# Kernel tuning notes

Hardware: AMD Instinct MI355X
Metric: run time of the kernel (lower is better)

Reference implementation:

```python
import jax, jax.numpy as jnp
import numpy as np

LN_EPS = 1e-5  # torch LayerNorm default
K_NN = 5       # top-5 nearest patterns (simple-surprise path)


def setup_inputs() -> dict:
    key = jax.random.key(0)
    ks = jax.random.split(key, 5)
    B, S, D, M = 8, 8192, 256, 50
    return {
        "hidden_states": jax.random.normal(ks[0], (B, S, D), dtype=jnp.float32),
        "memory": jax.random.normal(ks[1], (M, D), dtype=jnp.float32),
        "W1": jax.random.normal(ks[2], (D, 2 * D), dtype=jnp.float32) * (1.0 / np.sqrt(D)),
        "b1": jnp.zeros((2 * D,), dtype=jnp.float32),
        "W2": jax.random.normal(ks[3], (2 * D, D), dtype=jnp.float32) * (1.0 / np.sqrt(2 * D)),
        "b2": jnp.zeros((D,), dtype=jnp.float32),
        "ln_gamma": jnp.ones((D,), dtype=jnp.float32),
        "ln_beta": jnp.zeros((D,), dtype=jnp.float32),
    }


def reference(hidden_states, memory, W1, b1, W2, b2, ln_gamma, ln_beta):
    # Feature extractor: Linear -> ReLU -> (Dropout, eval=identity) -> Linear -> LayerNorm
    h = jax.nn.relu(jnp.einsum("bsd,de->bse", hidden_states, W1) + b1)
    f = jnp.einsum("bse,ed->bsd", h, W2) + b2
    mu = jnp.mean(f, axis=-1, keepdims=True)
    var = jnp.var(f, axis=-1, keepdims=True)
    feats = (f - mu) * jax.lax.rsqrt(var + LN_EPS) * ln_gamma + ln_beta  # [B,S,D]

    # Simple-surprise path, vectorized over all (b, s) tokens:
    # L2 distance of each token feature to every memory pattern.
    f_sq = jnp.sum(feats * feats, axis=-1)      # [B,S]
    m_sq = jnp.sum(memory * memory, axis=-1)    # [M]
    dots = jnp.einsum("bsd,md->bsm", feats, memory)  # [B,S,M]
    d2 = jnp.maximum(f_sq[..., None] + m_sq - 2.0 * dots, 0.0)
    dists = jnp.sqrt(d2)                        # [B,S,M]

    # k smallest distances -> mean -> sigmoid(avg - 1)
    neg_knn, _ = jax.lax.top_k(-dists, K_NN)    # [B,S,K]
    avg_dist = -jnp.mean(neg_knn, axis=-1)      # [B,S]
    surprise_scores = jax.nn.sigmoid(avg_dist - 1.0)
    return surprise_scores
```

## Files before the change

kernel.cpp:

```cpp
#include <hip/hip_runtime.h>
#include <math.h>

typedef __attribute__((ext_vector_type(8))) short bf16x8;
typedef __attribute__((ext_vector_type(4))) float f32x4;

static __device__ __forceinline__ unsigned short f2b(float x) {
  unsigned int u = __float_as_uint(x);
  u += 0x7FFFu + ((u >> 16) & 1u);
  return (unsigned short)(u >> 16);
}

__global__ void prep_weights(const float* __restrict__ W1,
                             const float* __restrict__ W2,
                             const float* __restrict__ mem,
                             unsigned short* __restrict__ W1T,
                             unsigned short* __restrict__ W2T,
                             unsigned short* __restrict__ memB,
                             float* __restrict__ msq) {
  int i = blockIdx.x * 256 + threadIdx.x;
  if (i < 131072) {
    int k = i >> 9, n = i & 511;
    W1T[n * 256 + k] = f2b(W1[i]);
  } else if (i < 262144) {
    int j = i - 131072;
    int k = j >> 8, n = j & 255;
    W2T[n * 512 + k] = f2b(W2[j]);
  } else if (i < 278528) {
    int j = i - 262144;
    int r = j >> 8;
    memB[j] = (r < 50) ? f2b(mem[j]) : (unsigned short)0;
  } else {
    int t = threadIdx.x;
    int r = t >> 2, c0 = (t & 3) * 64;
    float s = 0.f;
    if (r < 50) {
      for (int c = 0; c < 64; ++c) {
        float v = mem[r * 256 + c0 + c];
        s += v * v;
      }
    }
    s += __shfl_xor(s, 1, 64);
    s += __shfl_xor(s, 2, 64);
    if ((t & 3) == 0) msq[r] = (r < 50) ? s : 1e30f;
  }
}

#define DPitch 53

#define SWZ(b, r) ((b) ^ (((r) & 7) << 4))

__global__ __launch_bounds__(256, 4) void fused_main(
    const float* __restrict__ X, const float* __restrict__ b1v,
    const float* __restrict__ b2v, const float* __restrict__ gammav,
    const float* __restrict__ betav, const unsigned short* __restrict__ W1T,
    const unsigned short* __restrict__ W2T,
    const unsigned short* __restrict__ memB, const float* __restrict__ msq,
    float* __restrict__ out) {
  __shared__ __align__(16) char smem[40960];
  float* distS = (float*)smem;
  float* red = (float*)(smem + 32768);
  float* psum   = red;
  float* psumsq = red + 256;
  float* fsqp   = red + 512;
  float* muS    = red + 768;
  float* rstdS  = red + 832;
  float* fsqS   = red + 896;

  const char* W1Tc = (const char*)W1T;
  const char* W2Tc = (const char*)W2T;

  const int tid = threadIdx.x;
  const int wid = tid >> 6;
  const int lane = tid & 63;
  const int l16 = lane & 15;
  const int quad = lane >> 4;

  const float4* X4 = (const float4*)(X + (size_t)blockIdx.x * 64 * 256);
#pragma unroll
  for (int j = 0; j < 16; ++j) {
    int row = j * 4 + wid;
    float4 v = X4[row * 64 + lane];
    unsigned int p0 = f2b(v.x) | ((unsigned int)f2b(v.y) << 16);
    unsigned int p1 = f2b(v.z) | ((unsigned int)f2b(v.w) << 16);
    *(uint2*)(smem + SWZ(row * 512 + lane * 8, row)) = make_uint2(p0, p1);
  }

  f32x4 acc2[4][4];
#pragma unroll
  for (int mt = 0; mt < 4; ++mt) {
    const float4 bb = *(const float4*)(&b2v[wid * 64 + mt * 16 + quad * 4]);
#pragma unroll
    for (int nt = 0; nt < 4; ++nt) {
      acc2[mt][nt][0] = bb.x; acc2[mt][nt][1] = bb.y;
      acc2[mt][nt][2] = bb.z; acc2[mt][nt][3] = bb.w;
    }
  }

  __syncthreads();

  for (int cc = 0; cc < 8; ++cc) {
    int hbase = cc * 64 + wid * 16;
    f32x4 acc1[4];
    {
      const float4 bb = *(const float4*)(&b1v[hbase + quad * 4]);
#pragma unroll
      for (int nt = 0; nt < 4; ++nt) {
        acc1[nt][0] = bb.x; acc1[nt][1] = bb.y;
        acc1[nt][2] = bb.z; acc1[nt][3] = bb.w;
      }
    }
#pragma unroll
    for (int kk = 0; kk < 8; ++kk) {
      int kb = kk * 64 + quad * 16;
      bf16x8 a = *(const bf16x8*)(W1Tc + (hbase + l16) * 512 + kb);
      bf16x8 b[4];
#pragma unroll
      for (int nt = 0; nt < 4; ++nt) {
        int r = nt * 16 + l16;
        b[nt] = *(const bf16x8*)(smem + SWZ(r * 512 + kb, r));
      }
#pragma unroll
      for (int nt = 0; nt < 4; ++nt)
        acc1[nt] = __builtin_amdgcn_mfma_f32_16x16x32_bf16(a, b[nt], acc1[nt], 0, 0, 0);
    }
    __syncthreads();
#pragma unroll
    for (int nt = 0; nt < 4; ++nt) {
      int token = nt * 16 + l16;
      f32x4 v = acc1[nt];
      unsigned int p0 = f2b(fmaxf(v[0], 0.f)) | ((unsigned int)f2b(fmaxf(v[1], 0.f)) << 16);
      unsigned int p1 = f2b(fmaxf(v[2], 0.f)) | ((unsigned int)f2b(fmaxf(v[3], 0.f)) << 16);
      *(uint2*)(smem + 32768 + SWZ(token * 128 + wid * 32 + quad * 8, token)) =
          make_uint2(p0, p1);
    }
    __syncthreads();
#pragma unroll
    for (int k2 = 0; k2 < 2; ++k2) {
      bf16x8 a[4], b[4];
#pragma unroll
      for (int mt = 0; mt < 4; ++mt)
        a[mt] = *(const bf16x8*)(W2Tc + (wid * 64 + mt * 16 + l16) * 1024 +
                                 cc * 128 + k2 * 64 + quad * 16);
#pragma unroll
      for (int nt = 0; nt < 4; ++nt) {
        int r = nt * 16 + l16;
        b[nt] = *(const bf16x8*)(smem + 32768 + SWZ(r * 128 + k2 * 64 + quad * 16, r));
      }
#pragma unroll
      for (int mt = 0; mt < 4; ++mt)
#pragma unroll
        for (int nt = 0; nt < 4; ++nt)
          acc2[mt][nt] = __builtin_amdgcn_mfma_f32_16x16x32_bf16(
              a[mt], b[nt], acc2[mt][nt], 0, 0, 0);
    }
  }

  __syncthreads();

#pragma unroll
  for (int nt = 0; nt < 4; ++nt) {
    float s = 0.f, sq = 0.f;
#pragma unroll
    for (int mt = 0; mt < 4; ++mt)
#pragma unroll
      for (int r = 0; r < 4; ++r) {
        float v = acc2[mt][nt][r];
        s += v; sq += v * v;
      }
    s += __shfl_xor(s, 16, 64); sq += __shfl_xor(sq, 16, 64);
    s += __shfl_xor(s, 32, 64); sq += __shfl_xor(sq, 32, 64);
    if (quad == 0) {
      psum[wid * 64 + nt * 16 + l16] = s;
      psumsq[wid * 64 + nt * 16 + l16] = sq;
    }
  }
  __syncthreads();
  if (tid < 64) {
    float s = psum[tid] + psum[64 + tid] + psum[128 + tid] + psum[192 + tid];
    float sq = psumsq[tid] + psumsq[64 + tid] + psumsq[128 + tid] + psumsq[192 + tid];
    float mu = s * (1.f / 256.f);
    float var = sq * (1.f / 256.f) - mu * mu;
    muS[tid] = mu;
    rstdS[tid] = rsqrtf(var + 1e-5f);
  }
  __syncthreads();

  {
    float4 g[4], be[4];
#pragma unroll
    for (int mt = 0; mt < 4; ++mt) {
      g[mt]  = *(const float4*)(&gammav[wid * 64 + mt * 16 + quad * 4]);
      be[mt] = *(const float4*)(&betav[wid * 64 + mt * 16 + quad * 4]);
    }
#pragma unroll
    for (int nt = 0; nt < 4; ++nt) {
      int token = nt * 16 + l16;
      float mu = muS[token], rs = rstdS[token];
      float fs = 0.f;
#pragma unroll
      for (int mt = 0; mt < 4; ++mt) {
        float y0 = (acc2[mt][nt][0] - mu) * rs * g[mt].x + be[mt].x;
        float y1 = (acc2[mt][nt][1] - mu) * rs * g[mt].y + be[mt].y;
        float y2 = (acc2[mt][nt][2] - mu) * rs * g[mt].z + be[mt].z;
        float y3 = (acc2[mt][nt][3] - mu) * rs * g[mt].w + be[mt].w;
        fs += y0 * y0 + y1 * y1 + y2 * y2 + y3 * y3;
        unsigned int p0 = f2b(y0) | ((unsigned int)f2b(y1) << 16);
        unsigned int p1 = f2b(y2) | ((unsigned int)f2b(y3) << 16);
        *(uint2*)(smem + SWZ(token * 512 + wid * 128 + mt * 32 + quad * 8, token)) =
            make_uint2(p0, p1);
      }
      fs += __shfl_xor(fs, 16, 64);
      fs += __shfl_xor(fs, 32, 64);
      if (quad == 0) fsqp[wid * 64 + token] = fs;
    }
  }
  __syncthreads();
  if (tid < 64)
    fsqS[tid] = fsqp[tid] + fsqp[64 + tid] + fsqp[128 + tid] + fsqp[192 + tid];
  __syncthreads();

  f32x4 acc3[4];
#pragma unroll
  for (int nt = 0; nt < 4; ++nt) {
    acc3[nt][0] = 0.f; acc3[nt][1] = 0.f; acc3[nt][2] = 0.f; acc3[nt][3] = 0.f;
  }
#pragma unroll
  for (int kk = 0; kk < 8; ++kk) {
    int kb = kk * 64 + quad * 16;
    int ar = wid * 16 + l16;
    bf16x8 a = *(const bf16x8*)(smem + SWZ(ar * 512 + kb, ar));
    int k0 = kk * 32 + quad * 8;
#pragma unroll
    for (int nt = 0; nt < 4; ++nt) {
      bf16x8 b = *(const bf16x8*)(memB + (nt * 16 + l16) * 256 + k0);
      acc3[nt] = __builtin_amdgcn_mfma_f32_16x16x32_bf16(a, b, acc3[nt], 0, 0, 0);
    }
  }
  __syncthreads();
  {
    float4 fsq4 = *(const float4*)(&fsqS[wid * 16 + quad * 4]);
#pragma unroll
    for (int nt = 0; nt < 4; ++nt) {
      int col = nt * 16 + l16;
      float mq = msq[col];
#pragma unroll
      for (int r = 0; r < 4; ++r) {
        float fv = (r == 0) ? fsq4.x : (r == 1) ? fsq4.y : (r == 2) ? fsq4.z : fsq4.w;
        float d2 = fv + mq - 2.f * acc3[nt][r];
        float d = sqrtf(fmaxf(d2, 0.f));
        int row = wid * 16 + quad * 4 + r;
        if (col < 50) distS[row * DPitch + col] = d;
      }
    }
  }
  __syncthreads();

  if (tid < 64) {
    float b0 = 1e30f, b1 = 1e30f, b2 = 1e30f, b3 = 1e30f, b4 = 1e30f;
    const float* dr = &distS[tid * DPitch];
    for (int j = 0; j < 50; ++j) {
      float v = dr[j];
      b4 = fminf(b4, v);
      float t;
      if (b4 < b3) { t = b3; b3 = b4; b4 = t; }
      if (b3 < b2) { t = b2; b2 = b3; b3 = t; }
      if (b2 < b1) { t = b1; b1 = b2; b2 = t; }
      if (b1 < b0) { t = b0; b0 = b1; b1 = t; }
    }
    float avg = (b0 + b1 + b2 + b3 + b4) * 0.2f;
    float sarg = avg - 1.f;
    out[blockIdx.x * 64 + tid] = 1.f / (1.f + __expf(-sarg));
  }
}

extern "C" void kernel_launch(void* const* d_in, const int* in_sizes, int n_in,
                              void* d_out, int out_size, void* d_ws, size_t ws_size,
                              hipStream_t stream) {
  const float* X   = (const float*)d_in[0];
  const float* mem = (const float*)d_in[1];
  const float* W1  = (const float*)d_in[2];
  const float* b1  = (const float*)d_in[3];
  const float* W2  = (const float*)d_in[4];
  const float* b2  = (const float*)d_in[5];
  const float* g   = (const float*)d_in[6];
  const float* be  = (const float*)d_in[7];
  float* out = (float*)d_out;

  unsigned short* W1T  = (unsigned short*)d_ws;
  unsigned short* W2T  = W1T + 131072;
  unsigned short* memB = W2T + 131072;
  float* msq = (float*)(memB + 16384);

  prep_weights<<<1089, 256, 0, stream>>>(W1, W2, mem, W1T, W2T, memB, msq);
  fused_main<<<1024, 256, 0, stream>>>(X, b1, b2, g, be, W1T, W2T, memB, msq, out);
}
```

Before: 215.6 us.

## Double-buffer hidden chunks, widen chunk, use hardware bf16 pack conversion

The hidden-layer loop now runs in 4 chunks of 128 instead of 8 chunks of 64. Hidden activations are double-buffered in shared memory so the second GEMM for the previous chunk runs alongside the first GEMM of the current chunk, which leaves one barrier per chunk instead of two. Software bf16 rounding is replaced by the v_cvt_pk_bf16_f32 instruction. Shared memory grows to 64KB and launch bounds drop to 2 blocks per SM, so occupancy falls while register pressure rises.

Result: faster. 189.3 us (-12.2%).

```diff
diff --git a/kernel.cpp b/kernel.cpp
--- a/kernel.cpp
+++ b/kernel.cpp
@@ -8,6 +8,12 @@
   unsigned int u = __float_as_uint(x);
   u += 0x7FFFu + ((u >> 16) & 1u);
   return (unsigned short)(u >> 16);
+}
+
+static __device__ __forceinline__ unsigned int cvtpk(float lo, float hi) {
+  unsigned int r;
+  asm("v_cvt_pk_bf16_f32 %0, %1, %2" : "=v"(r) : "v"(lo), "v"(hi));
+  return r;
 }
 
 __global__ void prep_weights(const float* __restrict__ W1,
@@ -46,17 +52,16 @@
 }
 
 #define DPitch 53
-
 #define SWZ(b, r) ((b) ^ (((r) & 7) << 4))
 
-__global__ __launch_bounds__(256, 4) void fused_main(
+__global__ __launch_bounds__(256, 2) void fused_main(
     const float* __restrict__ X, const float* __restrict__ b1v,
     const float* __restrict__ b2v, const float* __restrict__ gammav,
     const float* __restrict__ betav, const unsigned short* __restrict__ W1T,
     const unsigned short* __restrict__ W2T,
     const unsigned short* __restrict__ memB, const float* __restrict__ msq,
     float* __restrict__ out) {
-  __shared__ __align__(16) char smem[40960];
+  __shared__ __align__(16) char smem[65536];
   float* distS = (float*)smem;
   float* red = (float*)(smem + 32768);
   float* psum   = red;
@@ -80,9 +85,8 @@
   for (int j = 0; j < 16; ++j) {
     int row = j * 4 + wid;
     float4 v = X4[row * 64 + lane];
-    unsigned int p0 = f2b(v.x) | ((unsigned int)f2b(v.y) << 16);
-    unsigned int p1 = f2b(v.z) | ((unsigned int)f2b(v.w) << 16);
-    *(uint2*)(smem + SWZ(row * 512 + lane * 8, row)) = make_uint2(p0, p1);
+    *(uint2*)(smem + SWZ(row * 512 + lane * 8, row)) =
+        make_uint2(cvtpk(v.x, v.y), cvtpk(v.z, v.w));
   }
 
   f32x4 acc2[4][4];
@@ -98,53 +102,90 @@
 
   __syncthreads();
 
-  for (int cc = 0; cc < 8; ++cc) {
-    int hbase = cc * 64 + wid * 16;
-    f32x4 acc1[4];
-    {
-      const float4 bb = *(const float4*)(&b1v[hbase + quad * 4]);
+#pragma unroll
+  for (int cc = 0; cc < 4; ++cc) {
+    if (cc > 0) {
+      const char* HsR = smem + 32768 + ((cc - 1) & 1) * 16384;
+#pragma unroll
+      for (int k2 = 0; k2 < 4; ++k2) {
+        bf16x8 a[4], b[4];
+#pragma unroll
+        for (int mt = 0; mt < 4; ++mt)
+          a[mt] = *(const bf16x8*)(W2Tc + (wid * 64 + mt * 16 + l16) * 1024 +
+                                   (cc - 1) * 256 + k2 * 64 + quad * 16);
+#pragma unroll
+        for (int nt = 0; nt < 4; ++nt) {
+          int r = nt * 16 + l16;
+          b[nt] = *(const bf16x8*)(HsR + SWZ(r * 256 + k2 * 64 + quad * 16, r));
+        }
+#pragma unroll
+        for (int mt = 0; mt < 4; ++mt)
+#pragma unroll
+          for (int nt = 0; nt < 4; ++nt)
+            acc2[mt][nt] = __builtin_amdgcn_mfma_f32_16x16x32_bf16(
+                a[mt], b[nt], acc2[mt][nt], 0, 0, 0);
+      }
+    }
+
+    int hbase = cc * 128 + wid * 32;
+    f32x4 acc1[2][4];
+#pragma unroll
+    for (int mt = 0; mt < 2; ++mt) {
+      const float4 bb = *(const float4*)(&b1v[hbase + mt * 16 + quad * 4]);
 #pragma unroll
       for (int nt = 0; nt < 4; ++nt) {
-        acc1[nt][0] = bb.x; acc1[nt][1] = bb.y;
-        acc1[nt][2] = bb.z; acc1[nt][3] = bb.w;
+        acc1[mt][nt][0] = bb.x; acc1[mt][nt][1] = bb.y;
+        acc1[mt][nt][2] = bb.z; acc1[mt][nt][3] = bb.w;
       }
     }
 #pragma unroll
     for (int kk = 0; kk < 8; ++kk) {
       int kb = kk * 64 + quad * 16;
-      bf16x8 a = *(const bf16x8*)(W1Tc + (hbase + l16) * 512 + kb);
-      bf16x8 b[4];
+      bf16x8 a[2], b[4];
+#pragma unroll
+      for (int mt = 0; mt < 2; ++mt)
+        a[mt] = *(const bf16x8*)(W1Tc + (hbase + mt * 16 + l16) * 512 + kb);
 #pragma unroll
       for (int nt = 0; nt < 4; ++nt) {
         int r = nt * 16 + l16;
         b[nt] = *(const bf16x8*)(smem + SWZ(r * 512 + kb, r));
       }
 #pragma unroll
-      for (int nt = 0; nt < 4; ++nt)
-        acc1[nt] = __builtin_amdgcn_mfma_f32_16x16x32_bf16(a, b[nt], acc1[nt], 0, 0, 0);
+      for (int mt = 0; mt < 2; ++mt)
+#pragma unroll
+        for (int nt = 0; nt < 4; ++nt)
+          acc1[mt][nt] = __builtin_amdgcn_mfma_f32_16x16x32_bf16(
+              a[mt], b[nt], acc1[mt][nt], 0, 0, 0);
+    }
+    {
+      char* HsW = smem + 32768 + (cc & 1) * 16384;
+#pragma unroll
+      for (int mt = 0; mt < 2; ++mt)
+#pragma unroll
+        for (int nt = 0; nt < 4; ++nt) {
+          int token = nt * 16 + l16;
+          f32x4 v = acc1[mt][nt];
+          *(uint2*)(HsW + SWZ(token * 256 + wid * 64 + mt * 32 + quad * 8, token)) =
+              make_uint2(cvtpk(fmaxf(v[0], 0.f), fmaxf(v[1], 0.f)),
+                         cvtpk(fmaxf(v[2], 0.f), fmaxf(v[3], 0.f)));
+        }
     }
     __syncthreads();
-#pragma unroll
-    for (int nt = 0; nt < 4; ++nt) {
-      int token = nt * 16 + l16;
-      f32x4 v = acc1[nt];
-      unsigned int p0 = f2b(fmaxf(v[0], 0.f)) | ((unsigned int)f2b(fmaxf(v[1], 0.f)) << 16);
-      unsigned int p1 = f2b(fmaxf(v[2], 0.f)) | ((unsigned int)f2b(fmaxf(v[3], 0.f)) << 16);
-      *(uint2*)(smem + 32768 + SWZ(token * 128 + wid * 32 + quad * 8, token)) =
-          make_uint2(p0, p1);
-    }
-    __syncthreads();
-#pragma unroll
-    for (int k2 = 0; k2 < 2; ++k2) {
+  }
+
+  {
+    const char* HsR = smem + 32768 + 16384;
+#pragma unroll
+    for (int k2 = 0; k2 < 4; ++k2) {
       bf16x8 a[4], b[4];
 #pragma unroll
       for (int mt = 0; mt < 4; ++mt)
         a[mt] = *(const bf16x8*)(W2Tc + (wid * 64 + mt * 16 + l16) * 1024 +
-                                 cc * 128 + k2 * 64 + quad * 16);
+                                 3 * 256 + k2 * 64 + quad * 16);
 #pragma unroll
       for (int nt = 0; nt < 4; ++nt) {
         int r = nt * 16 + l16;
-        b[nt] = *(const bf16x8*)(smem + 32768 + SWZ(r * 128 + k2 * 64 + quad * 16, r));
+        b[nt] = *(const bf16x8*)(HsR + SWZ(r * 256 + k2 * 64 + quad * 16, r));
       }
 #pragma unroll
       for (int mt = 0; mt < 4; ++mt)
@@ -154,8 +195,6 @@
               a[mt], b[nt], acc2[mt][nt], 0, 0, 0);
     }
   }
-
-  __syncthreads();
 
 #pragma unroll
   for (int nt = 0; nt < 4; ++nt) {
@@ -204,10 +243,8 @@
         float y2 = (acc2[mt][nt][2] - mu) * rs * g[mt].z + be[mt].z;
         float y3 = (acc2[mt][nt][3] - mu) * rs * g[mt].w + be[mt].w;
         fs += y0 * y0 + y1 * y1 + y2 * y2 + y3 * y3;
-        unsigned int p0 = f2b(y0) | ((unsigned int)f2b(y1) << 16);
-        unsigned int p1 = f2b(y2) | ((unsigned int)f2b(y3) << 16);
         *(uint2*)(smem + SWZ(token * 512 + wid * 128 + mt * 32 + quad * 8, token)) =
-            make_uint2(p0, p1);
+            make_uint2(cvtpk(y0, y1), cvtpk(y2, y3));
       }
       fs += __shfl_xor(fs, 16, 64);
       fs += __shfl_xor(fs, 32, 64);
```
